# Performance work log

Measured on AMD Instinct MI355X. Metric: run time of the kernel, lower is better.

Reference implementation:

```python
import jax, jax.numpy as jnp
import numpy as np

N_HEAD = 16
D_MODEL = 1024


def setup_inputs() -> dict:
    key = jax.random.key(0)
    k1, k2, k3, k4, k5, k6 = jax.random.split(key, 6)
    B, S, D = 2, 2048, D_MODEL
    src = jax.random.normal(k1, (B, S, D), dtype=jnp.float32)
    attn_mask = jax.random.uniform(k2, (B, S, S), dtype=jnp.float32)
    # torch nn.Linear(d, 3d) / nn.Linear(d, d) params; stored as (in, out) for x @ W
    scale = 1.0 / np.sqrt(D)
    W_qkv = jax.random.uniform(k3, (D, 3 * D), dtype=jnp.float32, minval=-scale, maxval=scale)
    b_qkv = jax.random.uniform(k4, (3 * D,), dtype=jnp.float32, minval=-scale, maxval=scale)
    W_out = jax.random.uniform(k5, (D, D), dtype=jnp.float32, minval=-scale, maxval=scale)
    b_out = jax.random.uniform(k6, (D,), dtype=jnp.float32, minval=-scale, maxval=scale)
    return {"src": src, "attn_mask": attn_mask, "W_qkv": W_qkv, "b_qkv": b_qkv,
            "W_out": W_out, "b_out": b_out}


def reference(src, attn_mask, W_qkv, b_qkv, W_out, b_out):
    B, S, D = src.shape
    H = N_HEAD
    dh = D // H
    # broadcast mask [B,S,S] -> [B,1,S,S] (matches torch unsqueeze(1))
    mask = attn_mask[:, None, :, :]
    qkv = src @ W_qkv + b_qkv                      # [B,S,3D]
    q, k, v = jnp.split(qkv, 3, axis=-1)
    q = q.reshape(B, S, H, dh).transpose(0, 2, 1, 3)   # [B,H,S,dh]
    k = k.reshape(B, S, H, dh).transpose(0, 2, 1, 3)
    v = v.reshape(B, S, H, dh).transpose(0, 2, 1, 3)
    scores = jnp.einsum('bhqd,bhkd->bhqk', q, k) * (float(dh) ** -0.5)
    scores = scores * mask + (mask - 1.0) * 10000.0
    weights = jax.nn.softmax(scores, axis=-1)      # dropout_p=0 -> identity in eval/train
    out = jnp.einsum('bhqk,bhkd->bhqd', weights, v)
    out = out.transpose(0, 2, 1, 3).reshape(B, S, D)
    return out @ W_out + b_out
```

## Files before the change

### kernel.cpp

```cpp
#include <hip/hip_runtime.h>
#include <stdint.h>

#define SEQ    2048
#define DMODEL 1024

typedef __bf16 bf16x8 __attribute__((ext_vector_type(8)));
typedef float  f32x4  __attribute__((ext_vector_type(4)));

typedef __attribute__((address_space(1))) const void CGV;
typedef __attribute__((address_space(3))) void LDSV;

__device__ __forceinline__ void load_lds16(const void* g, void* l) {
    __builtin_amdgcn_global_load_lds((CGV*)g, (LDSV*)l, 16, 0, 0);
}

__global__ __launch_bounds__(256)
void transpose_f32_to_bf16(const float* __restrict__ in, __bf16* __restrict__ out,
                           int R, int C)
{
    __shared__ float tile[32][33];
    const int t  = threadIdx.x;
    const int tx = t & 31, ty = t >> 5;
    const int c0 = blockIdx.x * 32;
    const int r0 = blockIdx.y * 32;
#pragma unroll
    for (int i = 0; i < 4; ++i)
        tile[ty + i * 8][tx] = in[(size_t)(r0 + ty + i * 8) * C + c0 + tx];
    __syncthreads();
#pragma unroll
    for (int i = 0; i < 4; ++i)
        out[(size_t)(c0 + ty + i * 8) * R + r0 + tx] = (__bf16)tile[tx][ty + i * 8];
}

__global__ __launch_bounds__(256)
void convert_f32_to_bf16(const float* __restrict__ in, __bf16* __restrict__ out)
{
    const int i = (blockIdx.x * 256 + threadIdx.x) * 8;
    float4 a = *(const float4*)(in + i);
    float4 b = *(const float4*)(in + i + 4);
    __bf16 tmp[8] = { (__bf16)a.x, (__bf16)a.y, (__bf16)a.z, (__bf16)a.w,
                      (__bf16)b.x, (__bf16)b.y, (__bf16)b.z, (__bf16)b.w };
    *(uint4*)(out + i) = *(uint4*)tmp;
}

__global__ __launch_bounds__(256)
void transpose_v(const __bf16* __restrict__ in, __bf16* __restrict__ out)
{
    __shared__ __bf16 tile[32][34];
    const int t  = threadIdx.x;
    const int tx = t & 31, ty = t >> 5;
    const int s0 = blockIdx.x * 32;
    const int d0 = blockIdx.y * 32;
    const int bh = blockIdx.z;
    const __bf16* ip = in  + (size_t)bh * SEQ * 64;
    __bf16*       op = out + (size_t)bh * 64 * SEQ;
#pragma unroll
    for (int i = 0; i < 4; ++i)
        tile[ty + i * 8][tx] = ip[(size_t)(s0 + ty + i * 8) * 64 + d0 + tx];
    __syncthreads();
#pragma unroll
    for (int i = 0; i < 4; ++i)
        op[(size_t)(d0 + ty + i * 8) * SEQ + s0 + tx] = tile[tx][ty + i * 8];
}

template<bool A_IS_F32>
__global__ __launch_bounds__(256)
void gemm_kernel(const void* __restrict__ Av, const __bf16* __restrict__ Bt,
                 const float* __restrict__ bias,
                 __bf16* __restrict__ Cq, __bf16* __restrict__ Ck,
                 __bf16* __restrict__ Cv, float* __restrict__ Cplain,
                 int K, int N, int mode)
{
    __shared__ __attribute__((aligned(16))) __bf16 As[128][32];
    __shared__ __attribute__((aligned(16))) __bf16 Bs[128][32];

    const int t    = threadIdx.x;
    const int wave = __builtin_amdgcn_readfirstlane(t >> 6);
    const int lane = t & 63;
    const int l15  = lane & 15;
    const int quad = lane >> 4;
    const int wm   = (wave >> 1) * 64;
    const int wn   = (wave & 1) * 64;
    const int m0   = blockIdx.y * 128;
    const int n0   = blockIdx.x * 128;

    const int arow  = lane >> 2;
    const int akoff = (lane & 3) * 8;

    f32x4 acc[4][4] = {};

    for (int k0 = 0; k0 < K; k0 += 32) {
        __syncthreads();
        if (A_IS_F32) {
            const float* A = (const float*)Av;
            int row = t >> 1, kk = (t & 1) * 16;
            const float* srcp = A + (size_t)(m0 + row) * K + k0 + kk;
            float4 v0 = *(const float4*)(srcp);
            float4 v1 = *(const float4*)(srcp + 4);
            float4 v2 = *(const float4*)(srcp + 8);
            float4 v3 = *(const float4*)(srcp + 12);
            __bf16 tmp[16] = {
                (__bf16)v0.x, (__bf16)v0.y, (__bf16)v0.z, (__bf16)v0.w,
                (__bf16)v1.x, (__bf16)v1.y, (__bf16)v1.z, (__bf16)v1.w,
                (__bf16)v2.x, (__bf16)v2.y, (__bf16)v2.z, (__bf16)v2.w,
                (__bf16)v3.x, (__bf16)v3.y, (__bf16)v3.z, (__bf16)v3.w };
            *(uint4*)(&As[row][kk])     = *(uint4*)(tmp);
            *(uint4*)(&As[row][kk + 8]) = *(uint4*)(tmp + 8);
        } else {
            const __bf16* A = (const __bf16*)Av;
#pragma unroll
            for (int p = 0; p < 2; ++p) {
                int slab = (wave * 2 + p) * 16;
                const __bf16* g = A + (size_t)(m0 + slab + arow) * K + k0 + akoff;
                load_lds16(g, &As[slab][0]);
            }
        }
#pragma unroll
        for (int p = 0; p < 2; ++p) {
            int slab = (wave * 2 + p) * 16;
            const __bf16* g = Bt + (size_t)(n0 + slab + arow) * K + k0 + akoff;
            load_lds16(g, &Bs[slab][0]);
        }
        __syncthreads();

        bf16x8 af[4], bfr[4];
#pragma unroll
        for (int mi = 0; mi < 4; ++mi)
            af[mi] = *(const bf16x8*)(&As[wm + mi * 16 + l15][quad * 8]);
#pragma unroll
        for (int ni = 0; ni < 4; ++ni)
            bfr[ni] = *(const bf16x8*)(&Bs[wn + ni * 16 + l15][quad * 8]);
#pragma unroll
        for (int mi = 0; mi < 4; ++mi)
#pragma unroll
            for (int ni = 0; ni < 4; ++ni)
                acc[mi][ni] = __builtin_amdgcn_mfma_f32_16x16x32_bf16(
                    af[mi], bfr[ni], acc[mi][ni], 0, 0, 0);
    }

#pragma unroll
    for (int mi = 0; mi < 4; ++mi) {
        int rowb = m0 + wm + mi * 16 + quad * 4;
#pragma unroll
        for (int ni = 0; ni < 4; ++ni) {
            int col = n0 + wn + ni * 16 + l15;
            float bia = bias[col];
#pragma unroll
            for (int r = 0; r < 4; ++r) {
                float v = acc[mi][ni][r] + bia;
                int rr = rowb + r;
                if (mode == 0) {
                    int b = rr >> 11;
                    int s = rr & 2047;
                    int part = col >> 10;
                    int rem  = col & 1023;
                    int h = rem >> 6;
                    int d = rem & 63;
                    __bf16* dst = (part == 0) ? Cq : (part == 1) ? Ck : Cv;
                    dst[(((size_t)(b * 16 + h)) * SEQ + s) * 64 + d] = (__bf16)v;
                } else {
                    Cplain[(size_t)rr * N + col] = v;
                }
            }
        }
    }
}

__global__ __launch_bounds__(256, 4)
void attn_kernel(const __bf16* __restrict__ Q, const __bf16* __restrict__ Kb,
                 const __bf16* __restrict__ Vtg, const float* __restrict__ mask,
                 __bf16* __restrict__ Out)
{
    __shared__ __attribute__((aligned(16))) __bf16 Kt[2][64 * 64];
    __shared__ __attribute__((aligned(16))) __bf16 Vt[2][64 * 64];
    __shared__ __attribute__((aligned(16))) __bf16 Ps[4][16 * 64];

    const int t    = threadIdx.x;
    const int wave = __builtin_amdgcn_readfirstlane(t >> 6);
    const int lane = t & 63;
    const int l15  = lane & 15;
    const int quad = lane >> 4;
    const int swq  = lane & 7;
    const int bh   = blockIdx.x;
    const int b    = bh >> 4;
    const int h    = bh & 15;
    const int q0   = blockIdx.y * 64 + wave * 16;

    const __bf16* Qp  = Q   + (size_t)bh * SEQ * 64;
    const __bf16* Kp  = Kb  + (size_t)bh * SEQ * 64;
    const __bf16* Vtp = Vtg + (size_t)bh * 64 * SEQ;
    const float*  Mrow = mask + (size_t)b * SEQ * SEQ + (size_t)(q0 + l15) * SEQ + quad * 4;

    const int ch  = wave * 2;
    const int rw0 = ch * 8 + (lane >> 3);
    const int swz = ((lane & 7) ^ (lane >> 3)) * 8;
    const __bf16* kS0 = Kp  + (size_t)rw0 * 64 + swz;
    const __bf16* kS1 = Kp  + (size_t)(rw0 + 8) * 64 + swz;
    const __bf16* vS0 = Vtp + (size_t)rw0 * SEQ + swz;
    const __bf16* vS1 = Vtp + (size_t)(rw0 + 8) * SEQ + swz;

    bf16x8 qf[2];
#pragma unroll
    for (int ks = 0; ks < 2; ++ks)
        qf[ks] = *(const bf16x8*)(Qp + (size_t)(q0 + l15) * 64 + ks * 32 + quad * 8);

    f32x4 oacc[4] = {};
    float mrun = -1e30f, lrun = 0.f;

    load_lds16(kS0, &Kt[0][ch * 512]);
    load_lds16(kS1, &Kt[0][(ch + 1) * 512]);
    load_lds16(vS0, &Vt[0][ch * 512]);
    load_lds16(vS1, &Vt[0][(ch + 1) * 512]);
    f32x4 mk[4];
#pragma unroll
    for (int nb = 0; nb < 4; ++nb)
        mk[nb] = *(const f32x4*)(Mrow + nb * 16);

    const char* PsW = (const char*)&Ps[wave][0] + l15 * 128;

#pragma unroll 2
    for (int tt = 0; tt < SEQ / 64; ++tt) {
        const int key0 = tt * 64;
        const int keyn = (key0 + 64 <= SEQ - 64) ? key0 + 64 : SEQ - 64;
        const int cur  = tt & 1;
        const char* kcur = (const char*)&Kt[cur][0];
        const char* vcur = (const char*)&Vt[cur][0];
        __bf16* knxt = &Kt[cur ^ 1][0];
        __bf16* vnxt = &Vt[cur ^ 1][0];

        asm volatile("s_waitcnt vmcnt(0)" ::: "memory");
        __builtin_amdgcn_s_barrier();
        __builtin_amdgcn_sched_barrier(0);

        load_lds16(kS0 + (size_t)keyn * 64, knxt + ch * 512);
        load_lds16(kS1 + (size_t)keyn * 64, knxt + (ch + 1) * 512);
        load_lds16(vS0 + keyn, vnxt + ch * 512);
        load_lds16(vS1 + keyn, vnxt + (ch + 1) * 512);
        __builtin_amdgcn_sched_barrier(0);

        f32x4 sa[4];
#pragma unroll
        for (int nb = 0; nb < 4; ++nb) {
            const char* kb = kcur + (nb * 16 + l15) * 128;
            bf16x8 kf0 = *(const bf16x8*)(kb + (((quad) ^ swq) << 4));
            bf16x8 kf1 = *(const bf16x8*)(kb + (((4 + quad) ^ swq) << 4));
            f32x4 z = {};
            z = __builtin_amdgcn_mfma_f32_16x16x32_bf16(kf0, qf[0], z, 0, 0, 0);
            z = __builtin_amdgcn_mfma_f32_16x16x32_bf16(kf1, qf[1], z, 0, 0, 0);
            sa[nb] = z;
        }

#pragma unroll
        for (int nb = 0; nb < 4; ++nb)
#pragma unroll
            for (int r = 0; r < 4; ++r) {
                float m  = mk[nb][r];
                float tt2 = __fmaf_rn(0.125f, sa[nb][r], 10000.0f);
                sa[nb][r] = __fmaf_rn(m, tt2, -10000.0f);
            }
#pragma unroll
        for (int nb = 0; nb < 4; ++nb)
            mk[nb] = *(const f32x4*)(Mrow + keyn + nb * 16);

        float vmax = -1e30f;
#pragma unroll
        for (int nb = 0; nb < 4; ++nb)
#pragma unroll
            for (int r = 0; r < 4; ++r)
                vmax = fmaxf(vmax, sa[nb][r]);
        vmax = fmaxf(vmax, __shfl_xor(vmax, 16));
        vmax = fmaxf(vmax, __shfl_xor(vmax, 32));
        float mnew  = fmaxf(mrun, vmax);
        float alpha = __expf(mrun - mnew);
        mrun = mnew;

        float accs = 0.f;
#pragma unroll
        for (int nb = 0; nb < 4; ++nb)
#pragma unroll
            for (int r = 0; r < 4; ++r) {
                float p = __expf(sa[nb][r] - mnew);
                sa[nb][r] = p;
                accs += p;
            }
        accs += __shfl_xor(accs, 16);
        accs += __shfl_xor(accs, 32);
        lrun = lrun * alpha + accs;

#pragma unroll
        for (int nb = 0; nb < 4; ++nb) {
            union { __bf16 hh[4]; uint2 u; } pk;
            pk.hh[0] = (__bf16)sa[nb][0];
            pk.hh[1] = (__bf16)sa[nb][1];
            pk.hh[2] = (__bf16)sa[nb][2];
            pk.hh[3] = (__bf16)sa[nb][3];
            *(uint2*)(PsW + (((nb * 2 + (quad >> 1)) ^ swq) << 4) + (quad & 1) * 8) = pk.u;
        }
        asm volatile("s_waitcnt lgkmcnt(0)" ::: "memory");
        __builtin_amdgcn_sched_barrier(0);

        float a4[4];
#pragma unroll
        for (int r = 0; r < 4; ++r)
            a4[r] = __shfl(alpha, quad * 4 + r);
#pragma unroll
        for (int cb = 0; cb < 4; ++cb)
#pragma unroll
            for (int r = 0; r < 4; ++r)
                oacc[cb][r] *= a4[r];

        bf16x8 pf0 = *(const bf16x8*)(PsW + (((quad) ^ swq) << 4));
        bf16x8 pf1 = *(const bf16x8*)(PsW + (((4 + quad) ^ swq) << 4));

        __builtin_amdgcn_s_setprio(1);
#pragma unroll
        for (int cb = 0; cb < 4; ++cb) {
            const char* vb = vcur + (cb * 16 + l15) * 128;
            bf16x8 vf0 = *(const bf16x8*)(vb + (((quad) ^ swq) << 4));
            bf16x8 vf1 = *(const bf16x8*)(vb + (((4 + quad) ^ swq) << 4));
            oacc[cb] = __builtin_amdgcn_mfma_f32_16x16x32_bf16(pf0, vf0, oacc[cb], 0, 0, 0);
            oacc[cb] = __builtin_amdgcn_mfma_f32_16x16x32_bf16(pf1, vf1, oacc[cb], 0, 0, 0);
        }
        __builtin_amdgcn_s_setprio(0);
    }

    float l4[4];
#pragma unroll
    for (int r = 0; r < 4; ++r)
        l4[r] = __shfl(lrun, quad * 4 + r);
#pragma unroll
    for (int cb = 0; cb < 4; ++cb) {
#pragma unroll
        for (int r = 0; r < 4; ++r) {
            int qq = q0 + quad * 4 + r;
            float v = oacc[cb][r] / l4[r];
            Out[((size_t)(b * SEQ + qq)) * DMODEL + h * 64 + cb * 16 + l15] = (__bf16)v;
        }
    }
}

extern "C" void kernel_launch(void* const* d_in, const int* in_sizes, int n_in,
                              void* d_out, int out_size, void* d_ws, size_t ws_size,
                              hipStream_t stream)
{
    const float* src  = nullptr;
    const float* mask = nullptr;
    const float* Wqkv = nullptr;
    const float* bqkv = nullptr;
    const float* Wout = nullptr;
    const float* bout = nullptr;
    for (int i = 0; i < n_in; ++i) {
        switch (in_sizes[i]) {
            case 4194304: src  = (const float*)d_in[i]; break;
            case 8388608: mask = (const float*)d_in[i]; break;
            case 3145728: Wqkv = (const float*)d_in[i]; break;
            case 3072:    bqkv = (const float*)d_in[i]; break;
            case 1048576: Wout = (const float*)d_in[i]; break;
            case 1024:    bout = (const float*)d_in[i]; break;
        }
    }
    float* out = (float*)d_out;

    const size_t NE = (size_t)2 * 16 * SEQ * 64;
    __bf16* Qb     = (__bf16*)d_ws;
    __bf16* Kb     = Qb + NE;
    __bf16* Vb     = Kb + NE;
    __bf16* Vtg    = Vb + NE;
    __bf16* Wqkv_t = Vtg + NE;
    __bf16* Wout_t = Wqkv_t + (size_t)3072 * 1024;
    __bf16* Ao     = Vb;
    __bf16* SrcBf  = Vtg;

    transpose_f32_to_bf16<<<dim3(3072 / 32, 1024 / 32), 256, 0, stream>>>(
        Wqkv, Wqkv_t, 1024, 3072);
    transpose_f32_to_bf16<<<dim3(1024 / 32, 1024 / 32), 256, 0, stream>>>(
        Wout, Wout_t, 1024, 1024);

    convert_f32_to_bf16<<<dim3(4194304 / (256 * 8)), 256, 0, stream>>>(src, SrcBf);

    gemm_kernel<false><<<dim3(3072 / 128, 4096 / 128), 256, 0, stream>>>(
        (const void*)SrcBf, Wqkv_t, bqkv, Qb, Kb, Vb, nullptr, 1024, 3072, 0);

    transpose_v<<<dim3(SEQ / 32, 2, 32), 256, 0, stream>>>(Vb, Vtg);

    attn_kernel<<<dim3(32, SEQ / 64), 256, 0, stream>>>(Qb, Kb, Vtg, mask, Ao);

    gemm_kernel<false><<<dim3(1024 / 128, 4096 / 128), 256, 0, stream>>>(
        (const void*)Ao, Wout_t, bout, nullptr, nullptr, nullptr, out, 1024, 1024, 1);
}
```

Measured before the change: 262.9 us.

## Double-buffer GEMM LDS loads, use exp2 softmax with lazy rescaling

The GEMM now keeps two LDS buffers and prefetches the next K-slab while MFMAs run on the current one, with a single barrier per iteration. The attention softmax folds log2(e) into the scale and mask constants so it can call exp2 directly. Output rescaling is skipped unless some row's max grows by more than 8 in the log2 domain. The lazy rescale lets probabilities reach up to 2^8 before renormalizing, which adds a small precision risk in the bf16 P values. The unused f32 A path and its template parameter are removed.

Measured after the change: 259.3 us. About the same (-1.4%).

```diff
diff --git a/kernel.cpp b/kernel.cpp
--- a/kernel.cpp
+++ b/kernel.cpp
@@ -13,6 +13,8 @@
 __device__ __forceinline__ void load_lds16(const void* g, void* l) {
     __builtin_amdgcn_global_load_lds((CGV*)g, (LDSV*)l, 16, 0, 0);
 }
+
+__device__ __forceinline__ float fast_exp2(float x) { return __builtin_exp2f(x); }
 
 __global__ __launch_bounds__(256)
 void transpose_f32_to_bf16(const float* __restrict__ in, __bf16* __restrict__ out,
@@ -63,16 +65,15 @@
         op[(size_t)(d0 + ty + i * 8) * SEQ + s0 + tx] = tile[tx][ty + i * 8];
 }
 
-template<bool A_IS_F32>
 __global__ __launch_bounds__(256)
-void gemm_kernel(const void* __restrict__ Av, const __bf16* __restrict__ Bt,
+void gemm_kernel(const __bf16* __restrict__ A, const __bf16* __restrict__ Bt,
                  const float* __restrict__ bias,
                  __bf16* __restrict__ Cq, __bf16* __restrict__ Ck,
                  __bf16* __restrict__ Cv, float* __restrict__ Cplain,
                  int K, int N, int mode)
 {
-    __shared__ __attribute__((aligned(16))) __bf16 As[128][32];
-    __shared__ __attribute__((aligned(16))) __bf16 Bs[128][32];
+    __shared__ __attribute__((aligned(16))) __bf16 As[2][128][32];
+    __shared__ __attribute__((aligned(16))) __bf16 Bs[2][128][32];
 
     const int t    = threadIdx.x;
     const int wave = __builtin_amdgcn_readfirstlane(t >> 6);
@@ -89,54 +90,44 @@
 
     f32x4 acc[4][4] = {};
 
+#define GSTAGE(buf, kk)                                                        \
+    {                                                                          \
+        _Pragma("unroll")                                                      \
+        for (int p = 0; p < 2; ++p) {                                          \
+            int slab = (wave * 2 + p) * 16;                                    \
+            load_lds16(A  + (size_t)(m0 + slab + arow) * K + (kk) + akoff,     \
+                       &As[buf][slab][0]);                                     \
+            load_lds16(Bt + (size_t)(n0 + slab + arow) * K + (kk) + akoff,     \
+                       &Bs[buf][slab][0]);                                     \
+        }                                                                      \
+    }
+
+    GSTAGE(0, 0);
+    int cur = 0;
+#pragma unroll 2
     for (int k0 = 0; k0 < K; k0 += 32) {
-        __syncthreads();
-        if (A_IS_F32) {
-            const float* A = (const float*)Av;
-            int row = t >> 1, kk = (t & 1) * 16;
-            const float* srcp = A + (size_t)(m0 + row) * K + k0 + kk;
-            float4 v0 = *(const float4*)(srcp);
-            float4 v1 = *(const float4*)(srcp + 4);
-            float4 v2 = *(const float4*)(srcp + 8);
-            float4 v3 = *(const float4*)(srcp + 12);
-            __bf16 tmp[16] = {
-                (__bf16)v0.x, (__bf16)v0.y, (__bf16)v0.z, (__bf16)v0.w,
-                (__bf16)v1.x, (__bf16)v1.y, (__bf16)v1.z, (__bf16)v1.w,
-                (__bf16)v2.x, (__bf16)v2.y, (__bf16)v2.z, (__bf16)v2.w,
-                (__bf16)v3.x, (__bf16)v3.y, (__bf16)v3.z, (__bf16)v3.w };
-            *(uint4*)(&As[row][kk])     = *(uint4*)(tmp);
-            *(uint4*)(&As[row][kk + 8]) = *(uint4*)(tmp + 8);
-        } else {
-            const __bf16* A = (const __bf16*)Av;
-#pragma unroll
-            for (int p = 0; p < 2; ++p) {
-                int slab = (wave * 2 + p) * 16;
-                const __bf16* g = A + (size_t)(m0 + slab + arow) * K + k0 + akoff;
-                load_lds16(g, &As[slab][0]);
-            }
-        }
-#pragma unroll
-        for (int p = 0; p < 2; ++p) {
-            int slab = (wave * 2 + p) * 16;
-            const __bf16* g = Bt + (size_t)(n0 + slab + arow) * K + k0 + akoff;
-            load_lds16(g, &Bs[slab][0]);
-        }
-        __syncthreads();
+        asm volatile("s_waitcnt vmcnt(0)" ::: "memory");
+        __builtin_amdgcn_s_barrier();
+        __builtin_amdgcn_sched_barrier(0);
+        if (k0 + 32 < K) GSTAGE(cur ^ 1, k0 + 32);
+        __builtin_amdgcn_sched_barrier(0);
 
         bf16x8 af[4], bfr[4];
 #pragma unroll
         for (int mi = 0; mi < 4; ++mi)
-            af[mi] = *(const bf16x8*)(&As[wm + mi * 16 + l15][quad * 8]);
+            af[mi] = *(const bf16x8*)(&As[cur][wm + mi * 16 + l15][quad * 8]);
 #pragma unroll
         for (int ni = 0; ni < 4; ++ni)
-            bfr[ni] = *(const bf16x8*)(&Bs[wn + ni * 16 + l15][quad * 8]);
+            bfr[ni] = *(const bf16x8*)(&Bs[cur][wn + ni * 16 + l15][quad * 8]);
 #pragma unroll
         for (int mi = 0; mi < 4; ++mi)
 #pragma unroll
             for (int ni = 0; ni < 4; ++ni)
                 acc[mi][ni] = __builtin_amdgcn_mfma_f32_16x16x32_bf16(
                     af[mi], bfr[ni], acc[mi][ni], 0, 0, 0);
-    }
+        cur ^= 1;
+    }
+#undef GSTAGE
 
 #pragma unroll
     for (int mi = 0; mi < 4; ++mi) {
@@ -186,6 +177,9 @@
     const int h    = bh & 15;
     const int q0   = blockIdx.y * 64 + wave * 16;
 
+    const float C1 = 0.180336880f;
+    const float C2 = 14426.9502f;
+
     const __bf16* Qp  = Q   + (size_t)bh * SEQ * 64;
     const __bf16* Kp  = Kb  + (size_t)bh * SEQ * 64;
     const __bf16* Vtp = Vtg + (size_t)bh * 64 * SEQ;
@@ -254,9 +248,8 @@
         for (int nb = 0; nb < 4; ++nb)
 #pragma unroll
             for (int r = 0; r < 4; ++r) {
-                float m  = mk[nb][r];
-                float tt2 = __fmaf_rn(0.125f, sa[nb][r], 10000.0f);
-                sa[nb][r] = __fmaf_rn(m, tt2, -10000.0f);
+                float tt2 = __fmaf_rn(C1, sa[nb][r], C2);
+                sa[nb][r] = __fmaf_rn(mk[nb][r], tt2, -C2);
             }
 #pragma unroll
         for (int nb = 0; nb < 4; ++nb)
@@ -270,16 +263,29 @@
                 vmax = fmaxf(vmax, sa[nb][r]);
         vmax = fmaxf(vmax, __shfl_xor(vmax, 16));
         vmax = fmaxf(vmax, __shfl_xor(vmax, 32));
-        float mnew  = fmaxf(mrun, vmax);
-        float alpha = __expf(mrun - mnew);
-        mrun = mnew;
+
+        float alpha = 1.f;
+        if (__any(vmax > mrun + 8.f)) {
+            float mnew = fmaxf(mrun, vmax);
+            alpha = fast_exp2(mrun - mnew);
+            mrun = mnew;
+            float a4[4];
+#pragma unroll
+            for (int r = 0; r < 4; ++r)
+                a4[r] = __shfl(alpha, quad * 4 + r);
+#pragma unroll
+            for (int cb = 0; cb < 4; ++cb)
+#pragma unroll
+                for (int r = 0; r < 4; ++r)
+                    oacc[cb][r] *= a4[r];
+        }
 
         float accs = 0.f;
 #pragma unroll
         for (int nb = 0; nb < 4; ++nb)
 #pragma unroll
             for (int r = 0; r < 4; ++r) {
-                float p = __expf(sa[nb][r] - mnew);
+                float p = fast_exp2(sa[nb][r] - mrun);
                 sa[nb][r] = p;
                 accs += p;
             }
@@ -298,16 +304,6 @@
         }
         asm volatile("s_waitcnt lgkmcnt(0)" ::: "memory");
         __builtin_amdgcn_sched_barrier(0);
-
-        float a4[4];
-#pragma unroll
-        for (int r = 0; r < 4; ++r)
-            a4[r] = __shfl(alpha, quad * 4 + r);
-#pragma unroll
-        for (int cb = 0; cb < 4; ++cb)
-#pragma unroll
-            for (int r = 0; r < 4; ++r)
-                oacc[cb][r] *= a4[r];
 
         bf16x8 pf0 = *(const bf16x8*)(PsW + (((quad) ^ swq) << 4));
         bf16x8 pf1 = *(const bf16x8*)(PsW + (((4 + quad) ^ swq) << 4));
@@ -378,13 +374,13 @@
 
     convert_f32_to_bf16<<<dim3(4194304 / (256 * 8)), 256, 0, stream>>>(src, SrcBf);
 
-    gemm_kernel<false><<<dim3(3072 / 128, 4096 / 128), 256, 0, stream>>>(
-        (const void*)SrcBf, Wqkv_t, bqkv, Qb, Kb, Vb, nullptr, 1024, 3072, 0);
+    gemm_kernel<<<dim3(3072 / 128, 4096 / 128), 256, 0, stream>>>(
+        SrcBf, Wqkv_t, bqkv, Qb, Kb, Vb, nullptr, 1024, 3072, 0);
 
     transpose_v<<<dim3(SEQ / 32, 2, 32), 256, 0, stream>>>(Vb, Vtg);
 
     attn_kernel<<<dim3(32, SEQ / 64), 256, 0, stream>>>(Qb, Kb, Vtg, mask, Ao);
 
-    gemm_kernel<false><<<dim3(1024 / 128, 4096 / 128), 256, 0, stream>>>(
-        (const void*)Ao, Wout_t, bout, nullptr, nullptr, nullptr, out, 1024, 1024, 1);
-}
+    gemm_kernel<<<dim3(1024 / 128, 4096 / 128), 256, 0, stream>>>(
+        Ao, Wout_t, bout, nullptr, nullptr, nullptr, out, 1024, 1024, 1);
+}
```
